# Performance work log

Hardware: AMD Instinct MI355X
Metric: run time of the kernel (lower is better)

## Reference

```python
import jax, jax.numpy as jnp
import numpy as np

TEMP = 0.1
QUEUE_SIZE = 512
CUTOFF_KM = 25.0
EARTH_R_KM = 6371.0088


def _normalize(x, eps=1e-12):
    # F.normalize: x / max(||x||, eps)
    n = jnp.linalg.norm(x, axis=-1, keepdims=True)
    return x / jnp.maximum(n, eps)


def _haversine_km(g1, g2):
    # g1: (B,2) [lat,lon] degrees; g2: (S,2) -> (B,S) great-circle km
    r = jnp.pi / 180.0
    lat1 = g1[:, 0:1] * r
    lon1 = g1[:, 1:2] * r
    lat2 = g2[None, :, 0] * r
    lon2 = g2[None, :, 1] * r
    dlat = lat2 - lat1
    dlon = lon2 - lon1
    a = jnp.sin(dlat / 2) ** 2 + jnp.cos(lat1) * jnp.cos(lat2) * jnp.sin(dlon / 2) ** 2
    return 2.0 * EARTH_R_KM * jnp.arcsin(jnp.sqrt(jnp.clip(a, 0.0, 1.0)))


def setup_inputs() -> dict:
    key = jax.random.key(0)
    k = jax.random.split(key, 7)
    n_aug, B, D, S = 4, 256, 768, 65536
    V = jax.random.normal(k[0], (n_aug, B, D), jnp.float32)
    L = jax.random.normal(k[1], (B, D), jnp.float32)
    gps = jnp.concatenate([
        jax.random.uniform(k[2], (B, 1), jnp.float32, -90.0, 90.0),
        jax.random.uniform(k[3], (B, 1), jnp.float32, -180.0, 180.0)], axis=1)
    support_features = jax.random.normal(k[4], (S, D), jnp.float32)
    support_gps = jnp.concatenate([
        jax.random.uniform(k[5], (S, 1), jnp.float32, -90.0, 90.0),
        jax.random.uniform(k[6], (S, 1), jnp.float32, -180.0, 180.0)], axis=1)
    return {"V": V, "L": L, "gps": gps,
            "support_features": support_features, "support_gps": support_gps}


def reference(V, L, gps, support_features, support_gps):
    # org joint embedding always from V[0]; nearest neighbour over raw support feats
    org = _normalize(V[0] * L)                                   # (B,D)
    sim = org @ support_features.T                               # (B,S)
    nn_idx = jnp.argmax(sim, axis=1)                             # (B,)
    nn = _normalize(support_features[nn_idx])                    # (B,D)

    # augmented joints for j = 1..n_aug-1
    augs = _normalize(V[1:] * L[None])                           # (J,B,D)
    # numerator always uses V[1] (as in the original code), constant over j
    num = jnp.einsum('bd,bd->b', nn, augs[0]) / TEMP             # (B,)

    # in-batch denominator: sum_i exp(nn_b . aug_{j,i} / T)
    batch_den = jnp.exp(jnp.einsum('bd,jid->jbi', nn, augs) / TEMP).sum(axis=2)  # (J,B)

    # GPS-filtered negative queue: first QUEUE_SIZE support entries > 25 km away,
    # zero-padded (zero rows contribute exp(0) = 1, matching the torch code)
    mask = _haversine_km(gps, support_gps) > CUTOFF_KM           # (B,S)
    order = jnp.argsort(jnp.where(mask, 0, 1), axis=1)[:, :QUEUE_SIZE]  # stable: kept in original order
    valid = jnp.take_along_axis(mask, order, axis=1)             # (B,Q)
    qfeat = support_features[order] * valid[..., None]           # (B,Q,D)
    queue_den = jnp.exp(jnp.einsum('bd,bqd->bq', nn, qfeat) / TEMP).sum(axis=1)  # (B,)

    den = jnp.log(batch_den + queue_den[None, :])                # (J,B)
    loss = -(num[None, :] - den).sum() / V.shape[1]
    return loss
```

## Files before the change

### kernel.cpp

```cpp
#include <hip/hip_runtime.h>
#include <hip/hip_bf16.h>

#define B_ROWS 256
#define S_SUP  65536
#define D_DIM  768
#define QSZ    512
#define NCHUNK 12
#define CHUNK_BYTES 32768

typedef short bf16x8 __attribute__((ext_vector_type(8)));
typedef float f32x4  __attribute__((ext_vector_type(4)));

__device__ __forceinline__ bf16x8 cvt8(float4 a, float4 b) {
  bf16x8 r;
  r[0] = (short)(__float_as_uint(a.x) >> 16);
  r[1] = (short)(__float_as_uint(a.y) >> 16);
  r[2] = (short)(__float_as_uint(a.z) >> 16);
  r[3] = (short)(__float_as_uint(a.w) >> 16);
  r[4] = (short)(__float_as_uint(b.x) >> 16);
  r[5] = (short)(__float_as_uint(b.y) >> 16);
  r[6] = (short)(__float_as_uint(b.z) >> 16);
  r[7] = (short)(__float_as_uint(b.w) >> 16);
  return r;
}

__device__ __forceinline__ void gl_lds16(const void* g, void* l) {
  __builtin_amdgcn_global_load_lds(
      (const __attribute__((address_space(1))) unsigned int*)g,
      (__attribute__((address_space(3))) unsigned int*)l, 16, 0, 0);
}

__device__ __forceinline__ float block_sum(float v) {
  __shared__ float tmp[4];
  #pragma unroll
  for (int m = 32; m >= 1; m >>= 1) v += __shfl_xor(v, m, 64);
  __syncthreads();
  if ((threadIdx.x & 63) == 0) tmp[threadIdx.x >> 6] = v;
  __syncthreads();
  return tmp[0] + tmp[1] + tmp[2] + tmp[3];
}

__device__ __forceinline__ double block_sum_d(double v) {
  __shared__ double tmp[4];
  #pragma unroll
  for (int m = 32; m >= 1; m >>= 1) v += __shfl_xor(v, m, 64);
  __syncthreads();
  if ((threadIdx.x & 63) == 0) tmp[threadIdx.x >> 6] = v;
  __syncthreads();
  return tmp[0] + tmp[1] + tmp[2] + tmp[3];
}

__global__ __launch_bounds__(256) void init_kernel(unsigned long long* gmax, double* bden) {
  int t = threadIdx.x;
  gmax[t] = 0ull;
  for (int i = t; i < 3 * B_ROWS; i += 256) bden[i] = 0.0;
}

__global__ __launch_bounds__(256) void prep_kernel(const float* __restrict__ V,
                                                   const float* __restrict__ L,
                                                   unsigned short* __restrict__ orgb,
                                                   float* __restrict__ augs) {
  int jb = blockIdx.x;
  int j = jb >> 8, b = jb & 255;
  int tid = threadIdx.x;
  const float* v = V + ((size_t)j * B_ROWS + b) * D_DIM;
  const float* l = L + (size_t)b * D_DIM;
  float p[3]; float ssq = 0.f;
  #pragma unroll
  for (int i = 0; i < 3; ++i) {
    int k = tid + 256 * i;
    p[i] = v[k] * l[k];
    ssq += p[i] * p[i];
  }
  ssq = block_sum(ssq);
  float inv = 1.0f / fmaxf(sqrtf(ssq), 1e-12f);
  if (j == 0) {
    #pragma unroll
    for (int i = 0; i < 3; ++i) {
      int k = tid + 256 * i;
      unsigned short hv = (unsigned short)(__float_as_uint(p[i] * inv) >> 16);
      int c = k >> 6, kk = k & 63, jg = kk >> 3, e = kk & 7;
      orgb[c * 16384 + b * 64 + ((jg ^ (b & 7)) << 3) + e] = hv;
    }
  } else {
    float* dst = augs + ((size_t)(j - 1) * B_ROWS + b) * D_DIM;
    #pragma unroll
    for (int i = 0; i < 3; ++i) dst[tid + 256 * i] = p[i] * inv;
  }
}

__global__ __launch_bounds__(256) void sim_argmax_kernel(const unsigned short* __restrict__ orgb,
                                                         const float* __restrict__ sf,
                                                         unsigned long long* __restrict__ gmax) {
  const int tid  = threadIdx.x;
  const int w    = tid >> 6;
  const int lid  = tid & 63;
  const int quad = lid >> 4;
  const int r15  = lid & 15;
  const int s_col = blockIdx.x * 64 + w * 16 + r15;

  __shared__ __align__(16) char smem[CHUNK_BYTES];

  f32x4 acc[16];
  #pragma unroll
  for (int t = 0; t < 16; ++t) acc[t] = (f32x4){0.f, 0.f, 0.f, 0.f};

  const float* bp = sf + (size_t)s_col * D_DIM + quad * 8;
  const char* gsrc_base = (const char*)orgb;

  for (int c = 0; c < NCHUNK; ++c) {
    {
      const char* g = gsrc_base + c * CHUNK_BYTES + w * 8192 + lid * 16;
      char* ldst = smem + w * 8192;
      #pragma unroll
      for (int i = 0; i < 8; ++i)
        gl_lds16(g + i * 1024, ldst + i * 1024);
    }
    __syncthreads();

    #pragma unroll
    for (int k1 = 0; k1 < 2; ++k1) {
      int k0 = c * 64 + k1 * 32;
      float4 b0 = *(const float4*)(bp + k0);
      float4 b1 = *(const float4*)(bp + k0 + 4);
      bf16x8 bf = cvt8(b0, b1);
      int abase = r15 * 128 + (((k1 * 4 + quad) ^ (r15 & 7)) << 4);
      #pragma unroll
      for (int t = 0; t < 16; ++t) {
        bf16x8 af = *(const bf16x8*)(smem + abase + t * 2048);
        acc[t] = __builtin_amdgcn_mfma_f32_16x16x32_bf16(af, bf, acc[t], 0, 0, 0);
      }
    }
    __syncthreads();
  }

  __shared__ float smax[4 * 256];
  __shared__ int   sidx[4 * 256];
  #pragma unroll
  for (int t = 0; t < 16; ++t) {
    #pragma unroll
    for (int r = 0; r < 4; ++r) {
      float v = acc[t][r];
      int   idx = s_col;
      #pragma unroll
      for (int m = 1; m < 16; m <<= 1) {
        float ov = __shfl_xor(v, m, 64);
        int   oi = __shfl_xor(idx, m, 64);
        if (ov > v || (ov == v && oi < idx)) { v = ov; idx = oi; }
      }
      if (r15 == 0) {
        int b = 16 * t + 4 * quad + r;
        smax[w * 256 + b] = v;
        sidx[w * 256 + b] = idx;
      }
    }
  }
  __syncthreads();
  {
    int b = tid;
    float v = smax[b]; int idx = sidx[b];
    #pragma unroll
    for (int w2 = 1; w2 < 4; ++w2) {
      float ov = smax[w2 * 256 + b]; int oi = sidx[w2 * 256 + b];
      if (ov > v || (ov == v && oi < idx)) { v = ov; idx = oi; }
    }
    unsigned u = __float_as_uint(v);
    unsigned key = (u & 0x80000000u) ? ~u : (u | 0x80000000u);
    unsigned long long packed = ((unsigned long long)key << 32) |
                                (unsigned long long)(0xFFFFFFFFu - (unsigned)idx);
    atomicMax(gmax + b, packed);
  }
}

__global__ __launch_bounds__(256) void nn_kernel(const unsigned long long* __restrict__ gmax,
                                                 const float* __restrict__ sf,
                                                 const float* __restrict__ augs,
                                                 float* __restrict__ nn,
                                                 float* __restrict__ nnT,
                                                 float* __restrict__ num) {
  int b = blockIdx.x, tid = threadIdx.x;
  int idx = (int)(0xFFFFFFFFu - (unsigned)(gmax[b] & 0xFFFFFFFFull));
  const float* row = sf + (size_t)idx * D_DIM;
  float p[3]; float ssq = 0.f;
  #pragma unroll
  for (int i = 0; i < 3; ++i) { p[i] = row[tid + 256 * i]; ssq += p[i] * p[i]; }
  ssq = block_sum(ssq);
  float inv = 1.0f / fmaxf(sqrtf(ssq), 1e-12f);
  const float* a0 = augs + (size_t)b * D_DIM;
  float dot = 0.f;
  #pragma unroll
  for (int i = 0; i < 3; ++i) {
    int k = tid + 256 * i;
    float nv = p[i] * inv;
    nn[(size_t)b * D_DIM + k] = nv;
    nnT[(size_t)k * B_ROWS + b] = nv;
    dot += nv * a0[k];
  }
  dot = block_sum(dot);
  if (tid == 0) num[b] = dot * 10.0f;
}

__global__ __launch_bounds__(256) void bden_kernel(const float* __restrict__ augs,
                                                   const float* __restrict__ nnT,
                                                   double* __restrict__ bden) {
  int jc = blockIdx.x;
  int j = jc >> 6, c = jc & 63;
  int i0 = c * 4;
  __shared__ float s_aug[4 * D_DIM];
  const float* src = augs + ((size_t)j * B_ROWS + i0) * D_DIM;
  for (int idx = threadIdx.x; idx < 4 * D_DIM; idx += 256) s_aug[idx] = src[idx];
  __syncthreads();
  int b = threadIdx.x;
  float a0 = 0.f, a1 = 0.f, a2 = 0.f, a3 = 0.f;
  for (int k = 0; k < D_DIM; ++k) {
    float nv = nnT[(size_t)k * B_ROWS + b];
    a0 += nv * s_aug[k];
    a1 += nv * s_aug[D_DIM + k];
    a2 += nv * s_aug[2 * D_DIM + k];
    a3 += nv * s_aug[3 * D_DIM + k];
  }
  double v = exp((double)a0 * 10.0) + exp((double)a1 * 10.0) +
             exp((double)a2 * 10.0) + exp((double)a3 * 10.0);
  atomicAdd(&bden[j * B_ROWS + b], v);
}

__global__ __launch_bounds__(256) void queue_kernel(const float* __restrict__ gps,
                                                    const float* __restrict__ sgps,
                                                    const float* __restrict__ sf,
                                                    const float* __restrict__ nn,
                                                    double* __restrict__ qden) {
  int b = blockIdx.x, tid = threadIdx.x;
  int w = tid >> 6, lane = tid & 63;
  __shared__ int qidx[QSZ];
  __shared__ int s_count;
  __shared__ int s_wcnt[4];
  __shared__ __align__(16) float s_nn[D_DIM];
  __shared__ double s_gsum[16];
  for (int k = tid; k < D_DIM; k += 256) s_nn[k] = nn[(size_t)b * D_DIM + k];
  if (tid == 0) s_count = 0;
  __syncthreads();

  const float r = 0.017453292519943295f;
  float lat1 = gps[b * 2 + 0] * r, lon1 = gps[b * 2 + 1] * r;
  float cl1 = cosf(lat1);
  int base = 0;
  while (true) {
    int count = s_count;
    if (count >= QSZ || base >= S_SUP) break;
    int s = base + tid;
    float lat2 = sgps[s * 2 + 0] * r, lon2 = sgps[s * 2 + 1] * r;
    float sdlat = sinf((lat2 - lat1) * 0.5f);
    float sdlon = sinf((lon2 - lon1) * 0.5f);
    float a = sdlat * sdlat + cl1 * cosf(lat2) * sdlon * sdlon;
    a = fminf(fmaxf(a, 0.f), 1.f);
    float d = 2.0f * 6371.0088f * asinf(sqrtf(a));
    bool valid = d > 25.0f;

    unsigned long long m = __ballot(valid);
    int wc = __popcll(m);
    if (lane == 0) s_wcnt[w] = wc;
    __syncthreads();
    int wbase = count;
    for (int i = 0; i < w; ++i) wbase += s_wcnt[i];
    int pos = wbase + __popcll(m & ((1ull << lane) - 1ull));
    if (valid && pos < QSZ) qidx[pos] = s;
    __syncthreads();
    if (tid == 0) {
      int total = s_wcnt[0] + s_wcnt[1] + s_wcnt[2] + s_wcnt[3];
      s_count = min(QSZ, count + total);
    }
    base += 256;
    __syncthreads();
  }
  int count = s_count;

  int g  = lane >> 4;
  int l2 = lane & 15;
  double acc = 0.0;
  const float4* nn4 = (const float4*)s_nn;
  for (int q = w * 4 + g; q < count; q += 16) {
    const float4* row = (const float4*)(sf + (size_t)qidx[q] * D_DIM);
    float dot = 0.f;
    #pragma unroll
    for (int i = 0; i < 12; ++i) {
      float4 a = row[l2 + 16 * i];
      float4 nv = nn4[l2 + 16 * i];
      dot += a.x * nv.x + a.y * nv.y + a.z * nv.z + a.w * nv.w;
    }
    #pragma unroll
    for (int m2 = 8; m2 >= 1; m2 >>= 1) dot += __shfl_xor(dot, m2, 16);
    if (l2 == 0) acc += exp((double)dot * 10.0);
  }
  if (l2 == 0) s_gsum[w * 4 + g] = acc;
  __syncthreads();
  if (tid == 0) {
    double t = (double)(QSZ - count);
    #pragma unroll
    for (int i = 0; i < 16; ++i) t += s_gsum[i];
    qden[b] = t;
  }
}

__global__ __launch_bounds__(256) void loss_kernel(const float* __restrict__ num,
                                                   const double* __restrict__ bden,
                                                   const double* __restrict__ qden,
                                                   float* __restrict__ out) {
  int b = threadIdx.x;
  double q = qden[b];
  double n = (double)num[b];
  double t = 0.0;
  #pragma unroll
  for (int j = 0; j < 3; ++j) t += n - log(bden[j * B_ROWS + b] + q);
  t = block_sum_d(t);
  if (b == 0) out[0] = (float)(-t / 256.0);
}

extern "C" void kernel_launch(void* const* d_in, const int* in_sizes, int n_in,
                              void* d_out, int out_size, void* d_ws, size_t ws_size,
                              hipStream_t stream) {
  const float* V    = (const float*)d_in[0];
  const float* L    = (const float*)d_in[1];
  const float* gps  = (const float*)d_in[2];
  const float* sf   = (const float*)d_in[3];
  const float* sgps = (const float*)d_in[4];
  float* out = (float*)d_out;

  char* ws = (char*)d_ws;
  size_t off = 0;
  unsigned short* orgb = (unsigned short*)(ws + off); off += 393216;
  float* augs = (float*)(ws + off); off += 2359296;
  float* nn   = (float*)(ws + off); off += 786432;
  float* nnT  = (float*)(ws + off); off += 786432;
  float* num  = (float*)(ws + off); off += 1024;
  double* bden = (double*)(ws + off); off += 6144;
  double* qden = (double*)(ws + off); off += 2048;
  unsigned long long* gmax = (unsigned long long*)(ws + off); off += 2048;

  init_kernel<<<1, 256, 0, stream>>>(gmax, bden);
  prep_kernel<<<1024, 256, 0, stream>>>(V, L, orgb, augs);
  sim_argmax_kernel<<<S_SUP / 64, 256, 0, stream>>>(orgb, sf, gmax);
  nn_kernel<<<B_ROWS, 256, 0, stream>>>(gmax, sf, augs, nn, nnT, num);
  bden_kernel<<<192, 256, 0, stream>>>(augs, nnT, bden);
  queue_kernel<<<B_ROWS, 256, 0, stream>>>(gps, sgps, sf, nn, qden);
  loss_kernel<<<1, 256, 0, stream>>>(num, bden, qden, out);
}
```

Baseline: 433.4 us.

## Retile sim-argmax GEMM with 8 warps, LDS-staged support tile, smaller K chunks

The similarity/argmax kernel moves from 4 warps each reading support rows straight from global memory to 8 warps in a 4x2 grid. Each K-chunk now stages both the orgb tile (32-wide K) and the fp32 support tile in LDS through direct global-to-LDS loads, with new XOR swizzles, and prep_kernel writes orgb in the matching layout. Accumulators per thread drop from 16 to 8 to raise occupancy, and the atomicMax is skipped when the stored value is already larger. The cost is twice as many chunk iterations and barriers, each doing less MFMA work.

```diff
diff --git a/kernel.cpp b/kernel.cpp
--- a/kernel.cpp
+++ b/kernel.cpp
@@ -5,8 +5,9 @@
 #define S_SUP  65536
 #define D_DIM  768
 #define QSZ    512
-#define NCHUNK 12
-#define CHUNK_BYTES 32768
+#define NCHUNK 24
+#define ACH 16384
+#define BCH 8192
 
 typedef short bf16x8 __attribute__((ext_vector_type(8)));
 typedef float f32x4  __attribute__((ext_vector_type(4)));
@@ -79,8 +80,9 @@
     for (int i = 0; i < 3; ++i) {
       int k = tid + 256 * i;
       unsigned short hv = (unsigned short)(__float_as_uint(p[i] * inv) >> 16);
-      int c = k >> 6, kk = k & 63, jg = kk >> 3, e = kk & 7;
-      orgb[c * 16384 + b * 64 + ((jg ^ (b & 7)) << 3) + e] = hv;
+      int c = k >> 5, jg = (k >> 3) & 3, e = k & 7;
+      int slot = jg ^ ((b >> 1) & 3);
+      orgb[c * 8192 + b * 32 + slot * 8 + e] = hv;
     }
   } else {
     float* dst = augs + ((size_t)(j - 1) * B_ROWS + b) * D_DIM;
@@ -89,86 +91,108 @@
   }
 }
 
-__global__ __launch_bounds__(256) void sim_argmax_kernel(const unsigned short* __restrict__ orgb,
-                                                         const float* __restrict__ sf,
-                                                         unsigned long long* __restrict__ gmax) {
+__global__ __launch_bounds__(512, 8) void sim_argmax_kernel(const unsigned short* __restrict__ orgb,
+                                                            const float* __restrict__ sf,
+                                                            unsigned long long* __restrict__ gmax) {
   const int tid  = threadIdx.x;
   const int w    = tid >> 6;
   const int lid  = tid & 63;
   const int quad = lid >> 4;
   const int r15  = lid & 15;
-  const int s_col = blockIdx.x * 64 + w * 16 + r15;
-
-  __shared__ __align__(16) char smem[CHUNK_BYTES];
-
-  f32x4 acc[16];
-  #pragma unroll
-  for (int t = 0; t < 16; ++t) acc[t] = (f32x4){0.f, 0.f, 0.f, 0.f};
-
-  const float* bp = sf + (size_t)s_col * D_DIM + quad * 8;
-  const char* gsrc_base = (const char*)orgb;
+  const int wr   = w >> 1;
+  const int wc   = w & 1;
+  const int s0   = blockIdx.x * 64;
+
+  __shared__ __align__(16) char smem[ACH + BCH];
+
+  f32x4 acc[8];
+  #pragma unroll
+  for (int t = 0; t < 8; ++t) acc[t] = (f32x4){0.f, 0.f, 0.f, 0.f};
+
+  const char* abase_g = (const char*)orgb + w * 1024 + lid * 16;
+  {
+  }
+  const int bs   = tid >> 3;
+  const int gi   = (tid & 7) ^ (bs & 7);
+  const float* bbase_g = sf + (size_t)(s0 + bs) * D_DIM + gi * 4;
+  char* a_dst0 = smem + w * 1024;
+  char* a_dst1 = smem + 8192 + w * 1024;
+  char* b_dst  = smem + ACH + w * 1024;
+
+  const int m7    = r15 & 7;
+  const int aslot = (quad ^ ((r15 >> 1) & 3)) << 4;
+  const char* arow = smem + (64 * wr + r15) * 64 + aslot;
+  const char* brow0 = smem + ACH + (wc * 32 + r15) * 128;
+  const char* brow1 = brow0 + 16 * 128;
+  const int gg = quad * 2;
+  const int bo0 = ((gg    ) ^ m7) << 4;
+  const int bo1 = ((gg + 1) ^ m7) << 4;
 
   for (int c = 0; c < NCHUNK; ++c) {
     {
-      const char* g = gsrc_base + c * CHUNK_BYTES + w * 8192 + lid * 16;
-      char* ldst = smem + w * 8192;
+      const char* g = abase_g + c * ACH;
+      gl_lds16(g,        a_dst0);
+      gl_lds16(g + 8192, a_dst1);
+    }
+    gl_lds16(bbase_g + c * 32, b_dst);
+    __syncthreads();
+
+    float4 p0 = *(const float4*)(brow0 + bo0);
+    float4 p1 = *(const float4*)(brow0 + bo1);
+    bf16x8 bf0 = cvt8(p0, p1);
+    float4 q0 = *(const float4*)(brow1 + bo0);
+    float4 q1 = *(const float4*)(brow1 + bo1);
+    bf16x8 bf1 = cvt8(q0, q1);
+    #pragma unroll
+    for (int t = 0; t < 4; ++t) {
+      bf16x8 af = *(const bf16x8*)(arow + t * 1024);
+      acc[t * 2 + 0] = __builtin_amdgcn_mfma_f32_16x16x32_bf16(af, bf0, acc[t * 2 + 0], 0, 0, 0);
+      acc[t * 2 + 1] = __builtin_amdgcn_mfma_f32_16x16x32_bf16(af, bf1, acc[t * 2 + 1], 0, 0, 0);
+    }
+    __syncthreads();
+  }
+
+  float* smax = (float*)smem;
+  int*   sidx = (int*)(smem + 2048);
+  #pragma unroll
+  for (int t = 0; t < 4; ++t) {
+    #pragma unroll
+    for (int r = 0; r < 4; ++r) {
+      float bv; int bi;
       #pragma unroll
-      for (int i = 0; i < 8; ++i)
-        gl_lds16(g + i * 1024, ldst + i * 1024);
-    }
-    __syncthreads();
-
-    #pragma unroll
-    for (int k1 = 0; k1 < 2; ++k1) {
-      int k0 = c * 64 + k1 * 32;
-      float4 b0 = *(const float4*)(bp + k0);
-      float4 b1 = *(const float4*)(bp + k0 + 4);
-      bf16x8 bf = cvt8(b0, b1);
-      int abase = r15 * 128 + (((k1 * 4 + quad) ^ (r15 & 7)) << 4);
-      #pragma unroll
-      for (int t = 0; t < 16; ++t) {
-        bf16x8 af = *(const bf16x8*)(smem + abase + t * 2048);
-        acc[t] = __builtin_amdgcn_mfma_f32_16x16x32_bf16(af, bf, acc[t], 0, 0, 0);
-      }
-    }
-    __syncthreads();
-  }
-
-  __shared__ float smax[4 * 256];
-  __shared__ int   sidx[4 * 256];
-  #pragma unroll
-  for (int t = 0; t < 16; ++t) {
-    #pragma unroll
-    for (int r = 0; r < 4; ++r) {
-      float v = acc[t][r];
-      int   idx = s_col;
-      #pragma unroll
-      for (int m = 1; m < 16; m <<= 1) {
-        float ov = __shfl_xor(v, m, 64);
-        int   oi = __shfl_xor(idx, m, 64);
-        if (ov > v || (ov == v && oi < idx)) { v = ov; idx = oi; }
+      for (int n = 0; n < 2; ++n) {
+        float v = acc[t * 2 + n][r];
+        int idx = s0 + wc * 32 + n * 16 + r15;
+        #pragma unroll
+        for (int m = 1; m < 16; m <<= 1) {
+          float ov = __shfl_xor(v, m, 64);
+          int   oi = __shfl_xor(idx, m, 64);
+          if (ov > v || (ov == v && oi < idx)) { v = ov; idx = oi; }
+        }
+        if (n == 0) { bv = v; bi = idx; }
+        else if (v > bv || (v == bv && idx < bi)) { bv = v; bi = idx; }
       }
       if (r15 == 0) {
-        int b = 16 * t + 4 * quad + r;
-        smax[w * 256 + b] = v;
-        sidx[w * 256 + b] = idx;
+        int local = 16 * t + 4 * quad + r;
+        smax[w * 64 + local] = bv;
+        sidx[w * 64 + local] = bi;
       }
     }
   }
   __syncthreads();
-  {
+  if (tid < 256) {
     int b = tid;
-    float v = smax[b]; int idx = sidx[b];
-    #pragma unroll
-    for (int w2 = 1; w2 < 4; ++w2) {
-      float ov = smax[w2 * 256 + b]; int oi = sidx[w2 * 256 + b];
-      if (ov > v || (ov == v && oi < idx)) { v = ov; idx = oi; }
-    }
+    int wrb = b >> 6, local = b & 63;
+    float v  = smax[(wrb * 2) * 64 + local];
+    int  idx = sidx[(wrb * 2) * 64 + local];
+    float ov = smax[(wrb * 2 + 1) * 64 + local];
+    int   oi = sidx[(wrb * 2 + 1) * 64 + local];
+    if (ov > v || (ov == v && oi < idx)) { v = ov; idx = oi; }
     unsigned u = __float_as_uint(v);
     unsigned key = (u & 0x80000000u) ? ~u : (u | 0x80000000u);
     unsigned long long packed = ((unsigned long long)key << 32) |
                                 (unsigned long long)(0xFFFFFFFFu - (unsigned)idx);
-    atomicMax(gmax + b, packed);
+    if (packed > gmax[b]) atomicMax(gmax + b, packed);
   }
 }
 
@@ -338,7 +362,7 @@
 
   init_kernel<<<1, 256, 0, stream>>>(gmax, bden);
   prep_kernel<<<1024, 256, 0, stream>>>(V, L, orgb, augs);
-  sim_argmax_kernel<<<S_SUP / 64, 256, 0, stream>>>(orgb, sf, gmax);
+  sim_argmax_kernel<<<S_SUP / 64, 512, 0, stream>>>(orgb, sf, gmax);
   nn_kernel<<<B_ROWS, 256, 0, stream>>>(gmax, sf, augs, nn, nnT, num);
   bden_kernel<<<192, 256, 0, stream>>>(augs, nnT, bden);
   queue_kernel<<<B_ROWS, 256, 0, stream>>>(gps, sgps, sf, nn, qden);
```

New measurement: 403.3 us. 6.9% less time.

## Retile similarity argmax GEMM with 32x32 MFMA and LDS-staged support tiles

Applied to the files above, without the earlier changes.

Rewrites the similarity/argmax kernel to process 128 support rows per 512-thread block. Each wave now computes a 64x64 sub-tile with 32x32x16 bf16 MFMAs, and the support features are converted to bf16 and staged in swizzled LDS. Before, each lane loaded its B operand straight from global memory for a 16-column slice. The goal is more operand reuse per LDS read and fewer global re-reads of the query block. The query layout in prep is changed to match, with vectorized bf16x8 stores. The final atomicMax is skipped when the packed value is not larger, at the cost of a racy pre-read and extra LDS and register pressure.

```diff
diff --git a/kernel.cpp b/kernel.cpp
--- a/kernel.cpp
+++ b/kernel.cpp
@@ -5,11 +5,13 @@
 #define S_SUP  65536
 #define D_DIM  768
 #define QSZ    512
-#define NCHUNK 12
-#define CHUNK_BYTES 32768
+#define NCH    12
+#define ABYTES 32768
+#define BBYTES 16384
 
 typedef short bf16x8 __attribute__((ext_vector_type(8)));
 typedef float f32x4  __attribute__((ext_vector_type(4)));
+typedef float f32x16 __attribute__((ext_vector_type(16)));
 
 __device__ __forceinline__ bf16x8 cvt8(float4 a, float4 b) {
   bf16x8 r;
@@ -63,6 +65,7 @@
   int jb = blockIdx.x;
   int j = jb >> 8, b = jb & 255;
   int tid = threadIdx.x;
+  __shared__ float srow[D_DIM];
   const float* v = V + ((size_t)j * B_ROWS + b) * D_DIM;
   const float* l = L + (size_t)b * D_DIM;
   float p[3]; float ssq = 0.f;
@@ -76,11 +79,15 @@
   float inv = 1.0f / fmaxf(sqrtf(ssq), 1e-12f);
   if (j == 0) {
     #pragma unroll
-    for (int i = 0; i < 3; ++i) {
-      int k = tid + 256 * i;
-      unsigned short hv = (unsigned short)(__float_as_uint(p[i] * inv) >> 16);
-      int c = k >> 6, kk = k & 63, jg = kk >> 3, e = kk & 7;
-      orgb[c * 16384 + b * 64 + ((jg ^ (b & 7)) << 3) + e] = hv;
+    for (int i = 0; i < 3; ++i) srow[tid + 256 * i] = p[i] * inv;
+    __syncthreads();
+    if (tid < 96) {
+      int k0 = tid * 8;
+      float4 f0 = *(const float4*)&srow[k0];
+      float4 f1 = *(const float4*)&srow[k0 + 4];
+      bf16x8 hv = cvt8(f0, f1);
+      int c = k0 >> 6, g = (k0 >> 3) & 7;
+      *(bf16x8*)(orgb + c * 16384 + g * 2048 + b * 8) = hv;
     }
   } else {
     float* dst = augs + ((size_t)(j - 1) * B_ROWS + b) * D_DIM;
@@ -89,86 +96,109 @@
   }
 }
 
-__global__ __launch_bounds__(256) void sim_argmax_kernel(const unsigned short* __restrict__ orgb,
-                                                         const float* __restrict__ sf,
-                                                         unsigned long long* __restrict__ gmax) {
-  const int tid  = threadIdx.x;
-  const int w    = tid >> 6;
-  const int lid  = tid & 63;
-  const int quad = lid >> 4;
-  const int r15  = lid & 15;
-  const int s_col = blockIdx.x * 64 + w * 16 + r15;
-
-  __shared__ __align__(16) char smem[CHUNK_BYTES];
-
-  f32x4 acc[16];
-  #pragma unroll
-  for (int t = 0; t < 16; ++t) acc[t] = (f32x4){0.f, 0.f, 0.f, 0.f};
-
-  const float* bp = sf + (size_t)s_col * D_DIM + quad * 8;
-  const char* gsrc_base = (const char*)orgb;
-
-  for (int c = 0; c < NCHUNK; ++c) {
+__global__ __launch_bounds__(512, 4) void sim_argmax_kernel(const unsigned short* __restrict__ orgb,
+                                                            const float* __restrict__ sf,
+                                                            unsigned long long* __restrict__ gmax) {
+  const int tid = threadIdx.x;
+  const int w   = tid >> 6;
+  const int l   = tid & 63;
+  const int h   = l >> 5;
+  const int c31 = l & 31;
+  const int wr  = w >> 1;
+  const int wc  = w & 1;
+  const int s0  = blockIdx.x * 128;
+
+  __shared__ __align__(16) char smem[ABYTES + BBYTES];
+
+  f32x16 acc[4];
+  #pragma unroll
+  for (int t = 0; t < 4; ++t)
+    #pragma unroll
+    for (int r = 0; r < 16; ++r) acc[t][r] = 0.f;
+
+  const int bs = tid >> 2;
+  const int ko = (tid & 3) * 16;
+  const float* bsrc0 = sf + (size_t)(s0 + bs) * D_DIM + ko;
+  const int g0 = ko >> 3;
+  char* bw0 = smem + ABYTES + g0 * 2048 + ((bs ^ g0) & 127) * 16;
+  char* bw1 = smem + ABYTES + (g0 + 1) * 2048 + ((bs ^ (g0 + 1)) & 127) * 16;
+
+  const char* agbase = (const char*)orgb + w * 1024 + l * 16;
+  char* aldst0 = smem + 0 * 8192 + w * 1024;
+  char* aldst1 = smem + 1 * 8192 + w * 1024;
+  char* aldst2 = smem + 2 * 8192 + w * 1024;
+  char* aldst3 = smem + 3 * 8192 + w * 1024;
+
+  const int ar0 = wr * 64 + c31;
+  const int ar1 = ar0 + 32;
+  const int bs0 = wc * 64 + c31;
+  const int bs1 = bs0 + 32;
+
+  for (int c = 0; c < NCH; ++c) {
+    const float4* bp = (const float4*)(bsrc0 + c * 64);
+    float4 f0 = bp[0], f1 = bp[1], f2 = bp[2], f3 = bp[3];
     {
-      const char* g = gsrc_base + c * CHUNK_BYTES + w * 8192 + lid * 16;
-      char* ldst = smem + w * 8192;
+      const char* g = agbase + c * ABYTES;
+      gl_lds16(g,         aldst0);
+      gl_lds16(g +  8192, aldst1);
+      gl_lds16(g + 16384, aldst2);
+      gl_lds16(g + 24576, aldst3);
+    }
+    *(bf16x8*)bw0 = cvt8(f0, f1);
+    *(bf16x8*)bw1 = cvt8(f2, f3);
+    __syncthreads();
+
+    #pragma unroll
+    for (int ks = 0; ks < 4; ++ks) {
+      int g = ks * 2 + h;
+      bf16x8 a0 = *(const bf16x8*)(smem + g * 4096 + ar0 * 16);
+      bf16x8 a1 = *(const bf16x8*)(smem + g * 4096 + ar1 * 16);
+      bf16x8 b0 = *(const bf16x8*)(smem + ABYTES + g * 2048 + ((bs0 ^ g) & 127) * 16);
+      bf16x8 b1 = *(const bf16x8*)(smem + ABYTES + g * 2048 + ((bs1 ^ g) & 127) * 16);
+      acc[0] = __builtin_amdgcn_mfma_f32_32x32x16_bf16(a0, b0, acc[0], 0, 0, 0);
+      acc[1] = __builtin_amdgcn_mfma_f32_32x32x16_bf16(a0, b1, acc[1], 0, 0, 0);
+      acc[2] = __builtin_amdgcn_mfma_f32_32x32x16_bf16(a1, b0, acc[2], 0, 0, 0);
+      acc[3] = __builtin_amdgcn_mfma_f32_32x32x16_bf16(a1, b1, acc[3], 0, 0, 0);
+    }
+    __syncthreads();
+  }
+
+  float* smax = (float*)smem;
+  int*   sidx = (int*)(smem + 2048);
+  #pragma unroll
+  for (int t = 0; t < 2; ++t) {
+    #pragma unroll
+    for (int rg = 0; rg < 16; ++rg) {
+      float v0 = acc[t * 2 + 0][rg];
+      float v1 = acc[t * 2 + 1][rg];
+      int i0 = s0 + wc * 64 + c31;
+      int i1 = i0 + 32;
+      float v; int idx;
+      if (v1 > v0) { v = v1; idx = i1; } else { v = v0; idx = i0; }
       #pragma unroll
-      for (int i = 0; i < 8; ++i)
-        gl_lds16(g + i * 1024, ldst + i * 1024);
-    }
-    __syncthreads();
-
-    #pragma unroll
-    for (int k1 = 0; k1 < 2; ++k1) {
-      int k0 = c * 64 + k1 * 32;
-      float4 b0 = *(const float4*)(bp + k0);
-      float4 b1 = *(const float4*)(bp + k0 + 4);
-      bf16x8 bf = cvt8(b0, b1);
-      int abase = r15 * 128 + (((k1 * 4 + quad) ^ (r15 & 7)) << 4);
-      #pragma unroll
-      for (int t = 0; t < 16; ++t) {
-        bf16x8 af = *(const bf16x8*)(smem + abase + t * 2048);
-        acc[t] = __builtin_amdgcn_mfma_f32_16x16x32_bf16(af, bf, acc[t], 0, 0, 0);
-      }
-    }
-    __syncthreads();
-  }
-
-  __shared__ float smax[4 * 256];
-  __shared__ int   sidx[4 * 256];
-  #pragma unroll
-  for (int t = 0; t < 16; ++t) {
-    #pragma unroll
-    for (int r = 0; r < 4; ++r) {
-      float v = acc[t][r];
-      int   idx = s_col;
-      #pragma unroll
-      for (int m = 1; m < 16; m <<= 1) {
+      for (int m = 1; m < 32; m <<= 1) {
         float ov = __shfl_xor(v, m, 64);
         int   oi = __shfl_xor(idx, m, 64);
         if (ov > v || (ov == v && oi < idx)) { v = ov; idx = oi; }
       }
-      if (r15 == 0) {
-        int b = 16 * t + 4 * quad + r;
-        smax[w * 256 + b] = v;
-        sidx[w * 256 + b] = idx;
+      if (c31 == 0) {
+        int row = wr * 64 + t * 32 + (rg & 3) + 8 * (rg >> 2) + 4 * h;
+        smax[wc * 256 + row] = v;
+        sidx[wc * 256 + row] = idx;
       }
     }
   }
   __syncthreads();
-  {
+  if (tid < 256) {
     int b = tid;
-    float v = smax[b]; int idx = sidx[b];
-    #pragma unroll
-    for (int w2 = 1; w2 < 4; ++w2) {
-      float ov = smax[w2 * 256 + b]; int oi = sidx[w2 * 256 + b];
-      if (ov > v || (ov == v && oi < idx)) { v = ov; idx = oi; }
-    }
+    float v  = smax[b];       int idx = sidx[b];
+    float ov = smax[256 + b]; int oi  = sidx[256 + b];
+    if (ov > v || (ov == v && oi < idx)) { v = ov; idx = oi; }
     unsigned u = __float_as_uint(v);
     unsigned key = (u & 0x80000000u) ? ~u : (u | 0x80000000u);
     unsigned long long packed = ((unsigned long long)key << 32) |
                                 (unsigned long long)(0xFFFFFFFFu - (unsigned)idx);
-    atomicMax(gmax + b, packed);
+    if (packed > gmax[b]) atomicMax(gmax + b, packed);
   }
 }
 
@@ -257,8 +287,8 @@
     bool valid = d > 25.0f;
 
     unsigned long long m = __ballot(valid);
-    int wc = __popcll(m);
-    if (lane == 0) s_wcnt[w] = wc;
+    int wcnt = __popcll(m);
+    if (lane == 0) s_wcnt[w] = wcnt;
     __syncthreads();
     int wbase = count;
     for (int i = 0; i < w; ++i) wbase += s_wcnt[i];
@@ -338,7 +368,7 @@
 
   init_kernel<<<1, 256, 0, stream>>>(gmax, bden);
   prep_kernel<<<1024, 256, 0, stream>>>(V, L, orgb, augs);
-  sim_argmax_kernel<<<S_SUP / 64, 256, 0, stream>>>(orgb, sf, gmax);
+  sim_argmax_kernel<<<S_SUP / 128, 512, 0, stream>>>(orgb, sf, gmax);
   nn_kernel<<<B_ROWS, 256, 0, stream>>>(gmax, sf, augs, nn, nnT, num);
   bden_kernel<<<192, 256, 0, stream>>>(augs, nnT, bden);
   queue_kernel<<<B_ROWS, 256, 0, stream>>>(gps, sgps, sf, nn, qden);
```

Result: faster. 394.4 us (-9.0%).
